# Performance work log

Hardware: AMD Instinct MI355X
Metric: run time of the kernel (lower is better)

## Reference

```python
import jax, jax.numpy as jnp
import numpy as np

N, E, F, C = 100000, 1600000, 64, 256


def setup_inputs() -> dict:
    key = jax.random.key(0)
    ks = jax.random.split(key, 9)

    def lin(k, fi, fo):
        kw, kb = jax.random.split(k)
        w = jax.random.normal(kw, (fi, fo), jnp.float32) * np.float32(1.0 / np.sqrt(fi))
        b = jax.random.normal(kb, (fo,), jnp.float32) * 0.001
        return w, b

    content = jax.random.normal(ks[0], (N, C), jnp.float32)
    node_emb = jax.random.normal(ks[1], (N + 1, F), jnp.float32) * np.float32(1.0 / (100 * F))
    proj_w, proj_b = lin(ks[2], C, F)
    c0w1, c0b1 = lin(ks[3], 2 * F, 4 * F)   # first layer: inp=2F -> 4F
    c0w2, c0b2 = lin(ks[4], 4 * F, F)
    c1w1, c1b1 = lin(ks[5], 3 * F, 6 * F)   # prediction layer: inp=3F -> 6F
    c1w2, c1b2 = lin(ks[6], 6 * F, F)
    nid = jnp.arange(N, dtype=jnp.int32)
    src = jax.random.randint(ks[7], (E,), 0, N, dtype=jnp.int32)
    dst = jax.random.randint(ks[8], (E,), 0, N, dtype=jnp.int32)
    return dict(content=content, node_emb=node_emb, proj_w=proj_w, proj_b=proj_b,
                c0w1=c0w1, c0b1=c0b1, c0w2=c0w2, c0b2=c0b2,
                c1w1=c1w1, c1b1=c1b1, c1w2=c1w2, c1b2=c1b2,
                nid=nid, src=src, dst=dst)


def _l2norm(x):
    # per-node L2 renorm with clamp(min=1e-6) like torch .norm().clamp
    n = jnp.linalg.norm(x, axis=1, keepdims=True)
    return x / jnp.maximum(n, 1e-6)


def _forward(content, node_emb, proj_w, proj_b,
             c0w1, c0b1, c0w2, c0b2, c1w1, c1b1, c1w2, c1b2,
             nid, src, dst):
    n = content.shape[0]
    lrelu = lambda x: jax.nn.leaky_relu(x, 0.1)
    # node init: embedding + projected content (GaussianNoise is identity in eval)
    h = node_emb[nid + 1] + lrelu(content @ proj_w + proj_b)
    # w = sum of 'one' over in-neighbors = in-degree
    deg = jax.ops.segment_sum(jnp.ones(src.shape[0], h.dtype), dst, num_segments=n)
    wden = jnp.maximum(deg - 1.0, 1.0)[:, None]  # (w - 1).clamp(min=1)

    # ---- layer 0 (first_layer) ----
    h_agg = jax.ops.segment_sum(h[src], dst, num_segments=n)  # copy_src('h') + sum
    h_agg = (h_agg - h) / wden
    z = lrelu(jnp.concatenate([h, h_agg], axis=1) @ c0w1 + c0b1)
    h_new = _l2norm(lrelu(z @ c0w2 + c0b2))
    h_res = _l2norm(h_agg)  # skip is None since in_dims == out_dims
    h = h_new

    # ---- layer 1 (prediction_layer) ----
    h_agg = jax.ops.segment_sum(h[src], dst, num_segments=n)
    h_res_sum = jax.ops.segment_sum(h_res[src], dst, num_segments=n)
    h_agg = (h_agg - h) / wden
    z = lrelu(jnp.concatenate([h, h_agg, h_res_sum], axis=1) @ c1w1 + c1b1)
    h_new = z @ c1w2 + c1b2  # prediction layer: no trailing LeakyReLU
    return _l2norm(h_new)


def reference(content, node_emb, proj_w, proj_b, c0w1, c0b1, c0w2, c0b2,
              c1w1, c1b1, c1w2, c1b2, nid, src, dst):
    return _forward(content, node_emb, proj_w, proj_b,
                    c0w1, c0b1, c0w2, c0b2, c1w1, c1b1, c1w2, c1b2,
                    nid, src, dst)
```

## Files before the change

### kernel.cpp

```cpp
#include <hip/hip_runtime.h>

typedef _Float16 half_t;
typedef half_t h8 __attribute__((ext_vector_type(8)));
typedef float f32x4 __attribute__((ext_vector_type(4)));
typedef unsigned int uint;
typedef unsigned long long ull;
typedef unsigned short ushort;

__device__ __forceinline__ float lrelu_f(float x){ return x >= 0.f ? x : 0.1f*x; }

__device__ __forceinline__ uint pack_h2(float a, float b){
  unsigned short lo = __builtin_bit_cast(unsigned short, (half_t)a);
  unsigned short hi = __builtin_bit_cast(unsigned short, (half_t)b);
  return (uint)lo | ((uint)hi << 16);
}
__device__ __forceinline__ h8 as_h8(uint4 v){ return __builtin_bit_cast(h8, v); }

__device__ __forceinline__ void acc_mix(float& lo, float& hi, uint pk, float one){
  asm("v_fma_mix_f32 %0, %1, %2, %0 op_sel:[0,0,0] op_sel_hi:[1,0,0]" : "+v"(lo) : "v"(pk), "v"(one));
  asm("v_fma_mix_f32 %0, %1, %2, %0 op_sel:[1,0,0] op_sel_hi:[1,0,0]" : "+v"(hi) : "v"(pk), "v"(one));
}

enum { EPI_INIT=0, EPI_LRELU=1, EPI_LRELU_L2=2, EPI_L2=3 };
constexpr int CAP = 64;
constexpr int CHUNK = 4096;
constexpr int OSTR = 1056;

__global__ __launch_bounds__(256) void front_kernel(
    const float* __restrict__ s0, half_t* __restrict__ d0,
    const float* __restrict__ s1, half_t* __restrict__ d1,
    const float* __restrict__ s2, half_t* __restrict__ d2,
    const float* __restrict__ s3, half_t* __restrict__ d3,
    const float* __restrict__ s4, half_t* __restrict__ d4,
    const int* __restrict__ src, const int* __restrict__ dst,
    ull* __restrict__ staging, ushort* __restrict__ offs, int E, int nbkt)
{
  __shared__ int hist[1024];
  __shared__ int cursor[1024];
  int b = blockIdx.x;

  if (b < 80){
    const float* w; half_t* o; int K, M;
    if      (b < 8)  { w=s0; o=d0; K=256; M=64;  }
    else if (b < 24) { w=s1; o=d1; K=128; M=256; b-=8; }
    else if (b < 32) { w=s2; o=d2; K=256; M=64;  b-=24; }
    else if (b < 68) { w=s3; o=d3; K=192; M=384; b-=32; }
    else             { w=s4; o=d4; K=384; M=64;  b-=68; }
    int idx = b*256 + threadIdx.x;
    int total = (K/32)*(M/16)*64;
    if (idx >= total) return;
    int lane = idx & 63;
    int t = idx >> 6;
    int CBn = M/16;
    int cb = t % CBn;
    int s  = t / CBn;
    int k0 = s*32 + (lane>>4)*8;
    int c  = cb*16 + (lane&15);
    #pragma unroll
    for (int j=0;j<8;++j) o[(size_t)idx*8 + j] = (half_t)w[(size_t)(k0+j)*M + c];
    return;
  }

  int c = b - 80;
  int base = c * CHUNK;
  for (int j = threadIdx.x; j < 1024; j += 256) hist[j] = 0;
  __syncthreads();
  #pragma unroll
  for (int it=0; it<CHUNK/256; ++it){
    int i = base + it*256 + threadIdx.x;
    if (i < E) atomicAdd(&hist[dst[i] >> 7], 1);
  }
  __syncthreads();
  for (int off=1; off<1024; off<<=1){
    int v[4];
    #pragma unroll
    for (int k=0;k<4;++k){
      int j = threadIdx.x + k*256;
      v[k] = (j>=off)? hist[j-off] : 0;
    }
    __syncthreads();
    #pragma unroll
    for (int k=0;k<4;++k) hist[threadIdx.x + k*256] += v[k];
    __syncthreads();
  }
  for (int j = threadIdx.x; j < 1024; j += 256){
    int ex = j ? hist[j-1] : 0;
    cursor[j] = ex;
    if (j <= nbkt) offs[(size_t)c*OSTR + j] = (ushort)ex;
  }
  __syncthreads();
  #pragma unroll
  for (int it=0; it<CHUNK/256; ++it){
    int i = base + it*256 + threadIdx.x;
    if (i < E){
      int d = dst[i];
      int s = src[i];
      int pos = atomicAdd(&cursor[d >> 7], 1);
      staging[(size_t)c*CHUNK + pos] = ((ull)(uint)d << 32) | (uint)s;
    }
  }
}

__global__ __launch_bounds__(256) void scatB_kernel(const ull* __restrict__ staging,
    const ushort* __restrict__ offs, int* __restrict__ cnt, int* __restrict__ col,
    int nChunks, int n){
  __shared__ int lcnt[128];
  int b = blockIdx.x;
  int node0 = b << 7;
  if (threadIdx.x < 128) lcnt[threadIdx.x] = 0;
  __syncthreads();
  for (int c = threadIdx.x; c < nChunks; c += 256){
    const ushort* op = offs + (size_t)c*OSTR;
    int o0 = op[b], o1 = op[b+1];
    const ull* sp = staging + (size_t)c*CHUNK;
    for (int j = o0; j < o1; ++j){
      ull v = sp[j];
      int d = (int)(v >> 32);
      int s = (int)(uint)v;
      int r = atomicAdd(&lcnt[d & 127], 1);
      if (r < CAP) col[(size_t)d*CAP + r] = s;
    }
  }
  __syncthreads();
  if (threadIdx.x < 128){
    int node = node0 + threadIdx.x;
    if (node < n) cnt[node] = lcnt[threadIdx.x];
  }
}

__global__ __launch_bounds__(256) void gemm_kernel(
  const float* __restrict__ x0,
  const half_t* __restrict__ wp, const float* __restrict__ bias,
  half_t* __restrict__ outv,
  const float* __restrict__ emb, const int* __restrict__ nid, int n)
{
  const int lane = threadIdx.x & 63;
  const int wid  = threadIdx.x >> 6;
  const int row0 = blockIdx.x*64 + wid*16;
  const int arow = row0 + (lane & 15);
  const int arowc = arow < n ? arow : n-1;
  const int khi = (lane>>4)*8;

  f32x4 areg[16];
  #pragma unroll
  for (int s=0;s<8;++s){
    uint k0 = (uint)arowc*256u + (uint)(s*32 + khi);
    areg[2*s]   = *(const f32x4*)(x0 + k0);
    areg[2*s+1] = *(const f32x4*)(x0 + k0 + 4);
  }

  f32x4 acc[4];
  #pragma unroll
  for (int cb=0;cb<4;++cb) acc[cb] = (f32x4){0.f,0.f,0.f,0.f};

  #pragma unroll
  for (int s=0;s<8;++s){
    h8 af;
    #pragma unroll
    for (int j=0;j<4;++j){ af[j]=(half_t)areg[2*s][j]; af[j+4]=(half_t)areg[2*s+1][j]; }
    const h8* wrow = (const h8*)wp + (size_t)(s*4)*64 + lane;
    #pragma unroll
    for (int cb=0;cb<4;++cb){
      h8 bf = wrow[cb*64];
      acc[cb] = __builtin_amdgcn_mfma_f32_16x16x32_f16(af, bf, acc[cb], 0,0,0);
    }
  }

  const int cgrp = lane >> 4;
  const int ccol = lane & 15;
  #pragma unroll
  for (int r=0;r<4;++r){
    int R = row0 + cgrp*4 + r;
    if (R < n){
      #pragma unroll
      for (int cb=0;cb<4;++cb){
        float t = lrelu_f(acc[cb][r] + bias[cb*16+ccol]);
        t += emb[(size_t)(nid[R]+1)*64 + cb*16 + ccol];
        outv[(size_t)R*64 + cb*16 + ccol] = (half_t)t;
      }
    }
  }
}

template<int K1, int M1, int M2, int NSRC, int EPI2, bool OUTF16>
__global__ __launch_bounds__(256,4) void mlp_kernel(
  const half_t* __restrict__ x0, const half_t* __restrict__ x1, const half_t* __restrict__ x2,
  int st0, int st1, int st2,
  const half_t* __restrict__ wp1, const float* __restrict__ b1,
  const half_t* __restrict__ wp2, const float* __restrict__ b2,
  void* __restrict__ outv, int ost, int n)
{
  constexpr int RS  = 17;
  constexpr int KS1 = K1/32, CBT = M1/16, CBW = CBT/4;
  constexpr int KS2 = M1/32, CB2 = M2/16;
  constexpr int RED = 65;
  __shared__ uint  zc[M1*RS];
  __shared__ float red[2*16*RED];

  const int lane = threadIdx.x & 63;
  const int wid  = threadIdx.x >> 6;
  const int row0 = blockIdx.x*32;
  const int khi  = (lane>>4)*8;
  const int ccol = lane & 15;
  const int cgrp = lane >> 4;

  f32x4 acc[2][CBW];
  #pragma unroll
  for (int t=0;t<2;++t)
    #pragma unroll
    for (int cb=0;cb<CBW;++cb) acc[t][cb] = (f32x4){0.f,0.f,0.f,0.f};

  #pragma unroll
  for (int s=0;s<KS1;++s){
    int k0 = s*32 + khi;
    const half_t* p = x0; int st = st0; int koff = k0;
    if constexpr (NSRC>1){
      int isrc = k0 >> 6;
      if constexpr (NSRC>=2){ if (isrc==1){ p=x1; st=st1; } }
      if constexpr (NSRC>=3){ if (isrc==2){ p=x2; st=st2; } }
      koff = k0 & 63;
    }
    h8 af[2];
    #pragma unroll
    for (int t=0;t<2;++t){
      int ar = row0 + t*16 + ccol; if (ar >= n) ar = n-1;
      af[t] = *(const h8*)(p + (size_t)ar*st + koff);
    }
    #pragma unroll
    for (int cb=0;cb<CBW;++cb){
      h8 bf = ((const h8*)wp1)[(size_t)(s*CBT + wid*CBW + cb)*64 + lane];
      #pragma unroll
      for (int t=0;t<2;++t)
        acc[t][cb] = __builtin_amdgcn_mfma_f32_16x16x32_f16(af[t], bf, acc[t][cb], 0,0,0);
    }
  }
  #pragma unroll
  for (int t=0;t<2;++t){
    #pragma unroll
    for (int cb=0;cb<CBW;++cb){
      int col = wid*(CBW*16) + cb*16 + ccol;
      float bb = b1[col];
      float v0 = lrelu_f(acc[t][cb][0]+bb);
      float v1 = lrelu_f(acc[t][cb][1]+bb);
      float v2 = lrelu_f(acc[t][cb][2]+bb);
      float v3 = lrelu_f(acc[t][cb][3]+bb);
      int idx = col*RS + t*8 + cgrp*2;
      zc[idx]   = pack_h2(v0,v1);
      zc[idx+1] = pack_h2(v2,v3);
    }
  }
  __syncthreads();

  const int rt = wid & 1, kh = wid >> 1;
  f32x4 acc2[CB2];
  #pragma unroll
  for (int cb=0;cb<CB2;++cb) acc2[cb] = (f32x4){0.f,0.f,0.f,0.f};
  const uint sel = (lane&1) ? 0x07060302u : 0x05040100u;
  const int rp0 = rt*8 + (ccol>>1);

  #pragma unroll
  for (int si=0;si<KS2/2;++si){
    int s = kh*(KS2/2) + si;
    uint v[8];
    #pragma unroll
    for (int j=0;j<8;++j) v[j] = zc[(s*32 + khi + j)*RS + rp0];
    uint4 u;
    u.x = __builtin_amdgcn_perm(v[1], v[0], sel);
    u.y = __builtin_amdgcn_perm(v[3], v[2], sel);
    u.z = __builtin_amdgcn_perm(v[5], v[4], sel);
    u.w = __builtin_amdgcn_perm(v[7], v[6], sel);
    h8 af2 = __builtin_bit_cast(h8, u);
    #pragma unroll
    for (int cb=0;cb<CB2;++cb){
      h8 bf = ((const h8*)wp2)[(size_t)(s*CB2+cb)*64 + lane];
      acc2[cb] = __builtin_amdgcn_mfma_f32_16x16x32_f16(af2, bf, acc2[cb], 0,0,0);
    }
  }
  if (kh == 1){
    #pragma unroll
    for (int cb=0;cb<CB2;++cb)
      #pragma unroll
      for (int r=0;r<4;++r)
        red[(rt*16 + cgrp*4 + r)*RED + cb*16 + ccol] = acc2[cb][r];
  }
  __syncthreads();
  if (kh == 0){
    #pragma unroll
    for (int r=0;r<4;++r){
      int Rr = row0 + rt*16 + cgrp*4 + r;
      float vv[CB2];
      #pragma unroll
      for (int cb=0;cb<CB2;++cb){
        float t = acc2[cb][r] + red[(rt*16 + cgrp*4 + r)*RED + cb*16 + ccol] + b2[cb*16+ccol];
        if constexpr (EPI2==EPI_LRELU_L2) t = lrelu_f(t);
        vv[cb] = t;
      }
      float sq = 0.f;
      #pragma unroll
      for (int cb=0;cb<CB2;++cb) sq += vv[cb]*vv[cb];
      sq += __shfl_xor(sq,1); sq += __shfl_xor(sq,2);
      sq += __shfl_xor(sq,4); sq += __shfl_xor(sq,8);
      float inv = 1.f / fmaxf(sqrtf(sq), 1e-6f);
      if (Rr < n){
        #pragma unroll
        for (int cb=0;cb<CB2;++cb){
          float t = vv[cb]*inv;
          if constexpr (OUTF16)
            ((half_t*)outv)[(size_t)Rr*ost + cb*16 + ccol] = (half_t)t;
          else
            ((float*)outv)[(size_t)Rr*ost + cb*16 + ccol] = t;
        }
      }
    }
  }
}

__global__ __launch_bounds__(256) void segsum0_kernel(const uint* __restrict__ hu, const int* __restrict__ cnt,
                               const int* __restrict__ col,
                               uint* __restrict__ hagg, uint* __restrict__ hc, int n){
  int node = blockIdx.x*4 + (threadIdx.x>>6);
  if (node >= n) return;
  int lane = threadIdx.x & 63;
  int g = lane >> 3, l = lane & 7;
  int deg = cnt[node];
  int degc = deg < CAP ? deg : CAP;
  const int* cv = col + ((uint)node<<6);
  const float one = 1.0f;
  float a[8] = {0,0,0,0,0,0,0,0};
  int j = g;
  for (; j + 8 < degc; j += 16){
    uint c0 = (uint)cv[j], c1 = (uint)cv[j+8];
    uint4 v0 = *(const uint4*)(hu + (c0<<5) + (l<<2));
    uint4 v1 = *(const uint4*)(hu + (c1<<5) + (l<<2));
    uint4 su = __builtin_bit_cast(uint4, as_h8(v0) + as_h8(v1));
    acc_mix(a[0],a[1],su.x,one); acc_mix(a[2],a[3],su.y,one);
    acc_mix(a[4],a[5],su.z,one); acc_mix(a[6],a[7],su.w,one);
  }
  if (j < degc){
    uint c = (uint)cv[j];
    uint4 v = *(const uint4*)(hu + (c<<5) + (l<<2));
    acc_mix(a[0],a[1],v.x,one); acc_mix(a[2],a[3],v.y,one);
    acc_mix(a[4],a[5],v.z,one); acc_mix(a[6],a[7],v.w,one);
  }
  #pragma unroll
  for (int q=0;q<8;++q){
    a[q] += __shfl_xor(a[q], 8);
    a[q] += __shfl_xor(a[q], 16);
    a[q] += __shfl_xor(a[q], 32);
  }
  uint4 hv4 = *(const uint4*)(hu + ((uint)node<<5) + (l<<2));
  h8 hvh = as_h8(hv4);
  float iwd = 1.f / fmaxf((float)deg - 1.f, 1.f);
  float sq = 0.f;
  #pragma unroll
  for (int q=0;q<8;++q){ a[q] = (a[q]-(float)hvh[q])*iwd; sq += a[q]*a[q]; }
  sq += __shfl_xor(sq,1); sq += __shfl_xor(sq,2); sq += __shfl_xor(sq,4);
  float inv = 1.f / fmaxf(sqrtf(sq), 1e-6f);
  if (g == 0){
    uint4 oa, oh;
    oa.x = pack_h2(a[0],a[1]); oa.y = pack_h2(a[2],a[3]);
    oa.z = pack_h2(a[4],a[5]); oa.w = pack_h2(a[6],a[7]);
    oh.x = pack_h2(a[0]*inv,a[1]*inv); oh.y = pack_h2(a[2]*inv,a[3]*inv);
    oh.z = pack_h2(a[4]*inv,a[5]*inv); oh.w = pack_h2(a[6]*inv,a[7]*inv);
    *(uint4*)(hagg + ((uint)node<<5) + (l<<2)) = oa;
    *(uint4*)(hc + ((uint)node<<6) + 32 + (l<<2)) = oh;
  }
}

__global__ __launch_bounds__(256) void segsum1_kernel(const uint* __restrict__ hcu, const int* __restrict__ cnt,
                               const int* __restrict__ col,
                               uint* __restrict__ hagg, uint* __restrict__ hsum, int n){
  int node = blockIdx.x*4 + (threadIdx.x>>6);
  if (node >= n) return;
  int lane = threadIdx.x & 63;
  int g = lane >> 4, l = lane & 15;
  int deg = cnt[node];
  int degc = deg < CAP ? deg : CAP;
  const int* cv = col + ((uint)node<<6);
  const float one = 1.0f;
  float a[8] = {0,0,0,0,0,0,0,0};
  int j = g;
  for (; j + 12 < degc; j += 16){
    uint c0 = (uint)cv[j], c1 = (uint)cv[j+4], c2 = (uint)cv[j+8], c3 = (uint)cv[j+12];
    uint4 v0 = *(const uint4*)(hcu + (c0<<6) + (l<<2));
    uint4 v1 = *(const uint4*)(hcu + (c1<<6) + (l<<2));
    uint4 v2 = *(const uint4*)(hcu + (c2<<6) + (l<<2));
    uint4 v3 = *(const uint4*)(hcu + (c3<<6) + (l<<2));
    uint4 su = __builtin_bit_cast(uint4, (as_h8(v0) + as_h8(v1)) + (as_h8(v2) + as_h8(v3)));
    acc_mix(a[0],a[1],su.x,one); acc_mix(a[2],a[3],su.y,one);
    acc_mix(a[4],a[5],su.z,one); acc_mix(a[6],a[7],su.w,one);
  }
  for (; j < degc; j += 4){
    uint c = (uint)cv[j];
    uint4 v = *(const uint4*)(hcu + (c<<6) + (l<<2));
    acc_mix(a[0],a[1],v.x,one); acc_mix(a[2],a[3],v.y,one);
    acc_mix(a[4],a[5],v.z,one); acc_mix(a[6],a[7],v.w,one);
  }
  #pragma unroll
  for (int q=0;q<8;++q){
    a[q] += __shfl_xor(a[q], 16);
    a[q] += __shfl_xor(a[q], 32);
  }
  if (g == 0){
    if (l < 8){
      uint4 hv4 = *(const uint4*)(hcu + ((uint)node<<6) + (l<<2));
      h8 hvh = as_h8(hv4);
      float iwd = 1.f / fmaxf((float)deg - 1.f, 1.f);
      uint4 o;
      o.x = pack_h2((a[0]-(float)hvh[0])*iwd,(a[1]-(float)hvh[1])*iwd);
      o.y = pack_h2((a[2]-(float)hvh[2])*iwd,(a[3]-(float)hvh[3])*iwd);
      o.z = pack_h2((a[4]-(float)hvh[4])*iwd,(a[5]-(float)hvh[5])*iwd);
      o.w = pack_h2((a[6]-(float)hvh[6])*iwd,(a[7]-(float)hvh[7])*iwd);
      *(uint4*)(hagg + ((uint)node<<5) + (l<<2)) = o;
    } else {
      uint4 o;
      o.x = pack_h2(a[0],a[1]); o.y = pack_h2(a[2],a[3]);
      o.z = pack_h2(a[4],a[5]); o.w = pack_h2(a[6],a[7]);
      *(uint4*)(hsum + ((uint)node<<5) + ((l-8)<<2)) = o;
    }
  }
}

extern "C" void kernel_launch(void* const* d_in, const int* in_sizes, int n_in,
                              void* d_out, int out_size, void* d_ws, size_t ws_size,
                              hipStream_t stream){
  const float* content = (const float*)d_in[0];
  const float* node_emb= (const float*)d_in[1];
  const float* proj_w  = (const float*)d_in[2];
  const float* proj_b  = (const float*)d_in[3];
  const float* c0w1 = (const float*)d_in[4];
  const float* c0b1 = (const float*)d_in[5];
  const float* c0w2 = (const float*)d_in[6];
  const float* c0b2 = (const float*)d_in[7];
  const float* c1w1 = (const float*)d_in[8];
  const float* c1b1 = (const float*)d_in[9];
  const float* c1w2 = (const float*)d_in[10];
  const float* c1b2 = (const float*)d_in[11];
  const int* nid = (const int*)d_in[12];
  const int* src = (const int*)d_in[13];
  const int* dst = (const int*)d_in[14];
  float* out = (float*)d_out;
  const int n = in_sizes[12];
  const int E = in_sizes[13];

  char* ws = (char*)d_ws;
  size_t off = 0;
  auto alloc = [&](size_t bytes)->char*{
    char* p = ws + off;
    off = (off + bytes + 255) & ~(size_t)255;
    return p;
  };
  const int nChunks = (E + CHUNK - 1)/CHUNK;
  const int nbkt = (n + 127) >> 7;
  half_t* h0   = (half_t*)alloc((size_t)n*64*2);
  half_t* hc   = (half_t*)alloc((size_t)n*128*2);
  half_t* hagg0= (half_t*)alloc((size_t)n*64*2);
  half_t* hagg1= (half_t*)alloc((size_t)n*64*2);
  half_t* hsum1= (half_t*)alloc((size_t)n*64*2);
  int* cnt    = (int*)alloc((size_t)n*4);
  int* col    = (int*)alloc((size_t)n*CAP*4);
  ull* staging= (ull*)alloc((size_t)nChunks*CHUNK*8);
  ushort* offs= (ushort*)alloc((size_t)nChunks*OSTR*2);
  half_t* wp0 = (half_t*)alloc((size_t)256*64*2);
  half_t* wp1 = (half_t*)alloc((size_t)128*256*2);
  half_t* wp2 = (half_t*)alloc((size_t)256*64*2);
  half_t* wp3 = (half_t*)alloc((size_t)192*384*2);
  half_t* wp4 = (half_t*)alloc((size_t)384*64*2);

  const int rgrid = (n + 63)/64;
  const int mgrid = (n + 31)/32;

  front_kernel<<<80 + nChunks, 256, 0, stream>>>(
      proj_w, wp0, c0w1, wp1, c0w2, wp2, c1w1, wp3, c1w2, wp4,
      src, dst, staging, offs, E, nbkt);

  scatB_kernel<<<nbkt,256,0,stream>>>(staging, offs, cnt, col, nChunks, n);

  gemm_kernel<<<rgrid,256,0,stream>>>(content, wp0, proj_b, h0, node_emb, nid, n);

  segsum0_kernel<<<(n+3)/4,256,0,stream>>>((const uint*)h0, cnt, col,
                                           (uint*)hagg0, (uint*)hc, n);
  mlp_kernel<128,256,64,2,EPI_LRELU_L2,true><<<mgrid,256,0,stream>>>(
      h0, hagg0, nullptr, 64,64,0, wp1, c0b1, wp2, c0b2, hc, 128, n);

  segsum1_kernel<<<(n+3)/4,256,0,stream>>>((const uint*)hc, cnt, col,
                                           (uint*)hagg1, (uint*)hsum1, n);
  mlp_kernel<192,384,64,3,EPI_L2,false><<<mgrid,256,0,stream>>>(
      hc, hagg1, hsum1, 128,64,64, wp3, c1b1, wp4, c1b2, out, 64, n);
}
```

Before: 273.0 us.

## Stage GEMM input rows through LDS with direct global-to-LDS loads

The projection GEMM now loads each block's 32 fp32 content rows into a swizzled LDS buffer using global_load_lds, which makes the row reads fully coalesced and avoids the 64-float register array per lane. Blocks shrink to 128 threads (2 waves, 32 rows) and the grid doubles. The XOR swizzle is meant to avoid LDS bank conflicts when the MFMA fragments are read back. The cost is 32KB of LDS per block, which limits occupancy, plus an extra barrier, and the first load and the compute no longer overlap.

```diff
diff --git a/kernel.cpp b/kernel.cpp
--- a/kernel.cpp
+++ b/kernel.cpp
@@ -128,36 +128,47 @@
   }
 }
 
-__global__ __launch_bounds__(256) void gemm_kernel(
+__global__ __launch_bounds__(128) void gemm_kernel(
   const float* __restrict__ x0,
   const half_t* __restrict__ wp, const float* __restrict__ bias,
   half_t* __restrict__ outv,
   const float* __restrict__ emb, const int* __restrict__ nid, int n)
 {
-  const int lane = threadIdx.x & 63;
-  const int wid  = threadIdx.x >> 6;
-  const int row0 = blockIdx.x*64 + wid*16;
-  const int arow = row0 + (lane & 15);
-  const int arowc = arow < n ? arow : n-1;
+  __shared__ float lds[32*256];
+  const int tid  = threadIdx.x;
+  const int lane = tid & 63;
+  const int wid  = tid >> 6;
+  const int row0 = blockIdx.x*32;
+
+  #pragma unroll
+  for (int r8 = 0; r8 < 16; ++r8){
+    int row = wid*16 + r8;
+    int grow = row0 + row; if (grow >= n) grow = n-1;
+    const char* gp = (const char*)(x0 + (size_t)grow*256)
+                   + ((((uint)lane*16u) ^ (((uint)row & 7u) << 4)));
+    __builtin_amdgcn_global_load_lds(
+        (__attribute__((address_space(1))) void*)gp,
+        (__attribute__((address_space(3))) void*)((char*)lds + row*1024),
+        16, 0, 0);
+  }
+  __syncthreads();
+
+  f32x4 acc[4];
+  #pragma unroll
+  for (int cb=0;cb<4;++cb) acc[cb] = (f32x4){0.f,0.f,0.f,0.f};
+
+  const int arow_l = wid*16 + (lane & 15);
+  const uint swz = ((uint)arow_l & 7u) << 4;
   const int khi = (lane>>4)*8;
 
-  f32x4 areg[16];
   #pragma unroll
   for (int s=0;s<8;++s){
-    uint k0 = (uint)arowc*256u + (uint)(s*32 + khi);
-    areg[2*s]   = *(const f32x4*)(x0 + k0);
-    areg[2*s+1] = *(const f32x4*)(x0 + k0 + 4);
-  }
-
-  f32x4 acc[4];
-  #pragma unroll
-  for (int cb=0;cb<4;++cb) acc[cb] = (f32x4){0.f,0.f,0.f,0.f};
-
-  #pragma unroll
-  for (int s=0;s<8;++s){
+    uint byte0 = (uint)(s*128 + khi*4);
+    f32x4 a0 = *(const f32x4*)((const char*)lds + arow_l*1024 + (byte0 ^ swz));
+    f32x4 a1 = *(const f32x4*)((const char*)lds + arow_l*1024 + ((byte0+16u) ^ swz));
     h8 af;
     #pragma unroll
-    for (int j=0;j<4;++j){ af[j]=(half_t)areg[2*s][j]; af[j+4]=(half_t)areg[2*s+1][j]; }
+    for (int j=0;j<4;++j){ af[j]=(half_t)a0[j]; af[j+4]=(half_t)a1[j]; }
     const h8* wrow = (const h8*)wp + (size_t)(s*4)*64 + lane;
     #pragma unroll
     for (int cb=0;cb<4;++cb){
@@ -170,7 +181,7 @@
   const int ccol = lane & 15;
   #pragma unroll
   for (int r=0;r<4;++r){
-    int R = row0 + cgrp*4 + r;
+    int R = row0 + wid*16 + cgrp*4 + r;
     if (R < n){
       #pragma unroll
       for (int cb=0;cb<4;++cb){
@@ -467,7 +478,7 @@
   half_t* wp3 = (half_t*)alloc((size_t)192*384*2);
   half_t* wp4 = (half_t*)alloc((size_t)384*64*2);
 
-  const int rgrid = (n + 63)/64;
+  const int ggrid = (n + 31)/32;
   const int mgrid = (n + 31)/32;
 
   front_kernel<<<80 + nChunks, 256, 0, stream>>>(
@@ -476,7 +487,7 @@
 
   scatB_kernel<<<nbkt,256,0,stream>>>(staging, offs, cnt, col, nChunks, n);
 
-  gemm_kernel<<<rgrid,256,0,stream>>>(content, wp0, proj_b, h0, node_emb, nid, n);
+  gemm_kernel<<<ggrid,128,0,stream>>>(content, wp0, proj_b, h0, node_emb, nid, n);
 
   segsum0_kernel<<<(n+3)/4,256,0,stream>>>((const uint*)h0, cnt, col,
                                            (uint*)hagg0, (uint*)hc, n);
```

New measurement: 278.7 us. 2.1% more time.
